# Kernel tuning notes

Measured on AMD Instinct MI355X. Metric: run time of the kernel, lower is better.

Reference implementation:

```python
import jax, jax.numpy as jnp
import numpy as np

B, S, H, DH, HQ, HKV = 2, 1024, 2048, 128, 16, 4
E, K, I, IS = 16, 4, 1024, 1024
EPS = 1e-5
ROPE_BASE = 10000.0
ROUTED_SCALE = 1.0


def rmsnorm(x, w):
    v = jnp.mean(x.astype(jnp.float32) ** 2, axis=-1, keepdims=True)
    return (x.astype(jnp.float32) * jax.lax.rsqrt(v + EPS)).astype(x.dtype) * w


def rope(x, cos, sin):
    x1, x2 = jnp.split(x, 2, axis=-1)
    return jnp.concatenate([x1 * cos - x2 * sin, x2 * cos + x1 * sin], axis=-1)


def setup_inputs() -> dict:
    key = jax.random.key(0)
    ks = jax.random.split(key, 24)
    s = 0.02
    inp = {}
    inp['x'] = jax.random.normal(ks[0], (B, S, H), dtype=jnp.float32)
    inp['in_ln_w'] = jnp.ones((H,), jnp.float32)
    inp['wq'] = jax.random.normal(ks[1], (H, HQ * DH), jnp.float32) * s
    inp['bq'] = jax.random.normal(ks[2], (HQ * DH,), jnp.float32) * s
    inp['wk'] = jax.random.normal(ks[3], (H, HKV * DH), jnp.float32) * s
    inp['bk'] = jax.random.normal(ks[4], (HKV * DH,), jnp.float32) * s
    inp['wv'] = jax.random.normal(ks[5], (H, HKV * DH), jnp.float32) * s
    inp['bv'] = jax.random.normal(ks[6], (HKV * DH,), jnp.float32) * s
    inp['qn_w'] = jnp.ones((DH,), jnp.float32)
    inp['kn_w'] = jnp.ones((DH,), jnp.float32)
    inp['wo'] = jax.random.normal(ks[7], (HQ * DH, H), jnp.float32) * s
    inp['post_ln_w'] = jnp.ones((H,), jnp.float32)
    inp['gate_w'] = jax.random.normal(ks[8], (E, H), jnp.float32) * s
    inp['gate_b'] = jax.random.normal(ks[9], (E,), jnp.float32) * s
    inp['wg'] = jax.random.normal(ks[10], (E, H, I), jnp.float32) * s
    inp['wu'] = jax.random.normal(ks[11], (E, H, I), jnp.float32) * s
    inp['wd'] = jax.random.normal(ks[12], (E, I, H), jnp.float32) * s
    inp['swg'] = jax.random.normal(ks[13], (H, IS), jnp.float32) * s
    inp['swu'] = jax.random.normal(ks[14], (H, IS), jnp.float32) * s
    inp['swd'] = jax.random.normal(ks[15], (IS, H), jnp.float32) * s
    return inp


def reference(x, in_ln_w, wq, bq, wk, bk, wv, bv, qn_w, kn_w, wo, post_ln_w,
              gate_w, gate_b, wg, wu, wd, swg, swu, swd):
    # ---- attention block ----
    res = x
    h = rmsnorm(x, in_ln_w)
    q = (h @ wq + bq).reshape(B, S, HQ, DH)
    k = (h @ wk + bk).reshape(B, S, HKV, DH)
    v = (h @ wv + bv).reshape(B, S, HKV, DH)
    q = rmsnorm(q, qn_w)  # per-head QK norm over head_dim
    k = rmsnorm(k, kn_w)
    inv_freq = 1.0 / (ROPE_BASE ** (jnp.arange(0, DH, 2, dtype=jnp.float32) / DH))  # [DH/2]
    fr = jnp.arange(S, dtype=jnp.float32)[:, None] * inv_freq[None, :]  # [S, DH/2]
    cos = jnp.cos(fr)[None, :, None, :]
    sin = jnp.sin(fr)[None, :, None, :]
    q = rope(q, cos, sin)
    k = rope(k, cos, sin)
    g = HQ // HKV
    k = jnp.repeat(k, g, axis=2)  # GQA expand to [B,S,HQ,DH]
    v = jnp.repeat(v, g, axis=2)
    scores = jnp.einsum('bqhd,bkhd->bhqk', q, k) * (DH ** -0.5)
    causal = jnp.tril(jnp.ones((S, S), dtype=bool))
    scores = jnp.where(causal[None, None], scores, jnp.float32(-1e30))
    attn = jax.nn.softmax(scores, axis=-1)
    o = jnp.einsum('bhqk,bkhd->bqhd', attn, v).reshape(B, S, HQ * DH) @ wo
    x = res + o
    # ---- MoE block ----
    res = x
    h = rmsnorm(x, post_ln_w)
    ht = h.reshape(B * S, H)  # [T, H]
    logits = ht.astype(jnp.float32) @ gate_w.T  # fp32 router
    scr = jax.nn.sigmoid(logits)  # [T, E]
    choice = scr + gate_b[None, :]  # noaux_tc: bias only for selection
    _, topi = jax.lax.top_k(choice, K)  # [T, K]
    tw = jnp.take_along_axis(scr, topi, axis=-1)  # unbiased combine weights
    tw = tw / (jnp.sum(tw, axis=-1, keepdims=True) + 1e-20)  # norm_topk_prob
    tw = tw * ROUTED_SCALE
    cw = jnp.sum(jax.nn.one_hot(topi, E, dtype=jnp.float32) * tw[..., None], axis=1)  # [T, E]
    a = jnp.einsum('th,ehi->eti', ht, wg)
    b = jnp.einsum('th,ehi->eti', ht, wu)
    inter = jax.nn.silu(a) * b * cw.T[:, :, None]  # scale before down-proj
    routed = jnp.einsum('eti,eih->th', inter, wd)
    shared = (jax.nn.silu(ht @ swg) * (ht @ swu)) @ swd
    out = res + (routed + shared).reshape(B, S, H)
    return out
```

## Files before the change

kernel.cpp:

```cpp
#include <hip/hip_runtime.h>
#include <math.h>

typedef unsigned short u16;
typedef __attribute__((ext_vector_type(8))) short short8;
typedef __attribute__((ext_vector_type(4))) float f32x4;

#define B_ 2
#define S_ 1024
#define H_ 2048
#define DH_ 128
#define HQ_ 16
#define HKV_ 4
#define E_ 16
#define TOPK_ 4
#define I_ 1024
#define T_ (B_*S_)
#define NQKV_ 3072
#define NSEG_ 17
#define NA_ (T_*TOPK_ + T_)
#define K3_ 6144

#define QPLANE ((long)B_*HQ_*S_*DH_)
#define KPLANE ((long)B_*HKV_*S_*DH_)
#define VPLANE ((long)B_*HKV_*DH_*S_)

__device__ __forceinline__ float bf2f(u16 u){
  union { unsigned int i; float f; } x; x.i = ((unsigned int)u) << 16; return x.f;
}
__device__ __forceinline__ u16 f2bf(float f){
  union { float f; unsigned int i; } x; x.f = f;
  unsigned int r = x.i + 0x7fffu + ((x.i >> 16) & 1u);
  return (u16)(r >> 16);
}
__device__ __forceinline__ void split_bf(float v, u16& hi, u16& lo){
  hi = f2bf(v);
  lo = f2bf(v - bf2f(hi));
}

__device__ __forceinline__ void gld_lds16(const void* g, void* l){
  __builtin_amdgcn_global_load_lds(
      (const __attribute__((address_space(1))) unsigned int*)g,
      (__attribute__((address_space(3))) unsigned int*)l, 16, 0, 0);
}

__device__ __forceinline__ f32x4 mfma_bf16(short8 a, short8 b, f32x4 c){
  return __builtin_amdgcn_mfma_f32_16x16x32_bf16(a, b, c, 0, 0, 0);
}

__global__ void k_transpose(const float* __restrict__ in, u16* __restrict__ out,
                            int R, int C, int rowMul, int rowOff,
                            long inBatch, long outBatch, int split3)
{
  __shared__ float tile[32][33];
  const float* inp = in + (long)blockIdx.z * inBatch;
  u16* outp = out + (long)blockIdx.z * outBatch;
  int c0 = blockIdx.x * 32, r0 = blockIdx.y * 32;
  int tx = threadIdx.x, ty = threadIdx.y;
#pragma unroll
  for (int i = 0; i < 4; i++)
    tile[ty*4+i][tx] = inp[(long)(r0 + ty*4 + i) * C + c0 + tx];
  __syncthreads();
#pragma unroll
  for (int i = 0; i < 4; i++){
    int c = c0 + ty*4 + i;
    float v = tile[tx][ty*4+i];
    if (split3){
      u16 hi, lo; split_bf(v, hi, lo);
      long base = (long)(c*rowMul + rowOff) * (3*R);
      outp[base + r0 + tx]       = hi;
      outp[base + R + r0 + tx]   = lo;
      outp[base + 2*R + r0 + tx] = hi;
    } else {
      outp[(long)(c*rowMul + rowOff) * R + r0 + tx] = f2bf(v);
    }
  }
}

__global__ void k_rmsnorm(const float* __restrict__ x, const float* __restrict__ w,
                          u16* __restrict__ out3, u16* __restrict__ out1,
                          float* __restrict__ outf)
{
  int t = blockIdx.x;
  const float4* r4 = (const float4*)(x + (long)t * H_);
  const float4* w4 = (const float4*)w;
  float4 a = r4[threadIdx.x], b = r4[threadIdx.x + 256];
  float ss = a.x*a.x + a.y*a.y + a.z*a.z + a.w*a.w
           + b.x*b.x + b.y*b.y + b.z*b.z + b.w*b.w;
#pragma unroll
  for (int d = 1; d < 64; d <<= 1) ss += __shfl_xor(ss, d);
  __shared__ float red[4];
  int lane = threadIdx.x & 63, wv = threadIdx.x >> 6;
  if (lane == 0) red[wv] = ss;
  __syncthreads();
  ss = red[0] + red[1] + red[2] + red[3];
  float rs = rsqrtf(ss * (1.f / 2048.f) + 1e-5f);
  float4 wa = w4[threadIdx.x], wb = w4[threadIdx.x + 256];
  float va[8] = { a.x*rs*wa.x, a.y*rs*wa.y, a.z*rs*wa.z, a.w*rs*wa.w,
                  b.x*rs*wb.x, b.y*rs*wb.y, b.z*rs*wb.z, b.w*rs*wb.w };
  int pos0 = threadIdx.x*4, pos1 = 1024 + threadIdx.x*4;
  if (out3){
    ushort4 hi0, lo0, hi1, lo1;
    split_bf(va[0], hi0.x, lo0.x); split_bf(va[1], hi0.y, lo0.y);
    split_bf(va[2], hi0.z, lo0.z); split_bf(va[3], hi0.w, lo0.w);
    split_bf(va[4], hi1.x, lo1.x); split_bf(va[5], hi1.y, lo1.y);
    split_bf(va[6], hi1.z, lo1.z); split_bf(va[7], hi1.w, lo1.w);
    u16* row = out3 + (long)t * K3_;
    *(ushort4*)(row + pos0) = hi0;        *(ushort4*)(row + pos1) = hi1;
    *(ushort4*)(row + 2048 + pos0) = hi0; *(ushort4*)(row + 2048 + pos1) = hi1;
    *(ushort4*)(row + 4096 + pos0) = lo0; *(ushort4*)(row + 4096 + pos1) = lo1;
  }
  if (out1){
    ushort4 p0 = { f2bf(va[0]), f2bf(va[1]), f2bf(va[2]), f2bf(va[3]) };
    ushort4 p1 = { f2bf(va[4]), f2bf(va[5]), f2bf(va[6]), f2bf(va[7]) };
    *(ushort4*)(out1 + (long)t*H_ + pos0) = p0;
    *(ushort4*)(out1 + (long)t*H_ + pos1) = p1;
  }
  if (outf){
    float4 oa = { va[0], va[1], va[2], va[3] };
    float4 ob = { va[4], va[5], va[6], va[7] };
    *(float4*)(outf + (long)t*H_ + pos0) = oa;
    *(float4*)(outf + (long)t*H_ + pos1) = ob;
  }
}

__global__ void k_ropetab(float* __restrict__ tab){
  int s = blockIdx.x, i = threadIdx.x;
  double inv = pow(10000.0, -(double)i / 64.0);
  double fr = (double)s * inv;
  tab[s*128 + i]      = (float)cos(fr);
  tab[s*128 + 64 + i] = (float)sin(fr);
}

__global__ void k_ropenorm(const float* __restrict__ qkv, const float* __restrict__ qnw,
                           const float* __restrict__ knw, const float* __restrict__ tab,
                           u16* __restrict__ Q, u16* __restrict__ Kn, u16* __restrict__ Vt)
{
  long gw = (long)blockIdx.x * 4 + (threadIdx.x >> 6);
  int lane = threadIdx.x & 63;
  int hr = (int)(gw % 24);
  long bs = gw / 24;
  int s = (int)(bs % S_);
  int b = (int)(bs / S_);
  const float* row = qkv + bs * NQKV_ + hr * DH_;
  float x1 = row[lane], x2 = row[lane + 64];
  if (hr < 20){
    float ss = x1*x1 + x2*x2;
#pragma unroll
    for (int d = 1; d < 64; d <<= 1) ss += __shfl_xor(ss, d);
    float rs = rsqrtf(ss * (1.f/128.f) + 1e-5f);
    const float* wn = (hr < 16) ? qnw : knw;
    float y1 = x1 * rs * wn[lane], y2 = x2 * rs * wn[lane + 64];
    float c = tab[s*128 + lane], sn = tab[s*128 + 64 + lane];
    float o1 = y1*c - y2*sn, o2 = y2*c + y1*sn;
    if (hr < 16){
      const float sc = 0.088388347648318447f;
      u16 h1,l1,h2,l2;
      split_bf(o1*sc, h1, l1); split_bf(o2*sc, h2, l2);
      u16* dst = Q + (((long)b*HQ_ + hr)*S_ + s) * DH_;
      dst[lane] = h1; dst[lane+64] = h2;
      dst[QPLANE + lane] = l1; dst[QPLANE + lane+64] = l2;
    } else {
      u16 h1,l1,h2,l2;
      split_bf(o1, h1, l1); split_bf(o2, h2, l2);
      u16* dst = Kn + (((long)b*HKV_ + (hr-16))*S_ + s) * DH_;
      dst[lane] = h1; dst[lane+64] = h2;
      dst[KPLANE + lane] = l1; dst[KPLANE + lane+64] = l2;
    }
  } else {
    u16 h1,l1,h2,l2;
    split_bf(x1, h1, l1); split_bf(x2, h2, l2);
    u16* dst = Vt + (((long)b*HKV_ + (hr-20))*DH_) * S_ + s;
    dst[(long)lane * S_]        = h1;
    dst[(long)(lane + 64) * S_] = h2;
    dst[VPLANE + (long)lane * S_]        = l1;
    dst[VPLANE + (long)(lane + 64) * S_] = l2;
  }
}

__launch_bounds__(256)
__global__ void k_attn(const u16* __restrict__ Q, const u16* __restrict__ Kn,
                       const u16* __restrict__ Vt, u16* __restrict__ O3)
{
  __shared__ u16 Ksh[32][128];
  __shared__ u16 Ksl[32][128];
  __shared__ u16 Vsh[128][32];
  __shared__ u16 Vsl[128][32];
  __shared__ u16 Psh[4][16][40];
  __shared__ u16 Psl[4][16][40];
  int qb = blockIdx.x, h = blockIdx.y, b = blockIdx.z;
  int kvh = h >> 2;
  int q0 = qb * 64;
  int tid = threadIdx.x, lane = tid & 63, w = tid >> 6;

  const u16* Qg = Q  + (((long)b*HQ_  + h  )*S_ + q0) * DH_;
  const u16* Kg = Kn + (((long)b*HKV_ + kvh)*S_) * DH_;
  const u16* Vg = Vt + (((long)b*HKV_ + kvh)*DH_) * S_;

  short8 qh[4], ql[4];
  {
    long qrow = w*16 + (lane & 15);
    int coff = (lane >> 4) << 3;
#pragma unroll
    for (int kst = 0; kst < 4; kst++){
      qh[kst] = *(const short8*)(Qg + qrow*DH_ + kst*32 + coff);
      ql[kst] = *(const short8*)(Qg + QPLANE + qrow*DH_ + kst*32 + coff);
    }
  }

  f32x4 o[8];
#pragma unroll
  for (int nt = 0; nt < 8; nt++) o[nt] = (f32x4){0.f,0.f,0.f,0.f};
  float mrow[4] = {-INFINITY,-INFINITY,-INFINITY,-INFINITY};
  float lrow[4] = {0.f,0.f,0.f,0.f};

  for (int j = 0; j <= 2*qb + 1; ++j){
#pragma unroll
    for (int it = 0; it < 2; ++it){
      int flat = it*256 + tid;
      int r = flat >> 4, pc = flat & 15;
      int c = pc ^ (((r&7) << 1) | ((r >> 3) & 1));
      long gsrc = ((long)(j*32 + r))*DH_ + c*8;
      gld_lds16(Kg + gsrc,          &Ksh[0][0] + (it*256 + (w<<6))*8);
      gld_lds16(Kg + KPLANE + gsrc, &Ksl[0][0] + (it*256 + (w<<6))*8);
    }
#pragma unroll
    for (int it = 0; it < 2; ++it){
      int flat = it*256 + tid;
      int r = flat >> 2, pc = flat & 3;
      int c = pc ^ (r & 3);
      long gsrc = (long)r*S_ + j*32 + c*8;
      gld_lds16(Vg + gsrc,          &Vsh[0][0] + (it*256 + (w<<6))*8);
      gld_lds16(Vg + VPLANE + gsrc, &Vsl[0][0] + (it*256 + (w<<6))*8);
    }
    __syncthreads();

    f32x4 s[2];
#pragma unroll
    for (int nt = 0; nt < 2; nt++) s[nt] = (f32x4){0.f,0.f,0.f,0.f};
#pragma unroll
    for (int kst = 0; kst < 4; kst++){
#pragma unroll
      for (int nt = 0; nt < 2; nt++){
        int br = nt*16 + (lane & 15);
        int bc = (kst*4 + (lane >> 4)) ^ (((br&7)<<1) | ((br>>3)&1));
        short8 kh = *(const short8*)&Ksh[br][bc*8];
        short8 kl = *(const short8*)&Ksl[br][bc*8];
        s[nt] = mfma_bf16(qh[kst], kh, s[nt]);
        s[nt] = mfma_bf16(qh[kst], kl, s[nt]);
        s[nt] = mfma_bf16(ql[kst], kh, s[nt]);
      }
    }
    if (j >= 2*qb){
#pragma unroll
      for (int nt = 0; nt < 2; nt++){
        int key = j*32 + nt*16 + (lane & 15);
#pragma unroll
        for (int r = 0; r < 4; r++){
          int qrow = q0 + w*16 + ((lane >> 4) << 2) + r;
          if (key > qrow) s[nt][r] = -1e30f;
        }
      }
    }
    float pm[4];
#pragma unroll
    for (int r = 0; r < 4; r++) pm[r] = fmaxf(s[0][r], s[1][r]);
#pragma unroll
    for (int d = 1; d < 16; d <<= 1){
#pragma unroll
      for (int r = 0; r < 4; r++) pm[r] = fmaxf(pm[r], __shfl_xor(pm[r], d));
    }
    float alpha[4];
#pragma unroll
    for (int r = 0; r < 4; r++){
      float mn = fmaxf(mrow[r], pm[r]);
      alpha[r] = __expf(mrow[r] - mn);
      mrow[r] = mn;
    }
    float psum[4] = {0.f,0.f,0.f,0.f};
#pragma unroll
    for (int nt = 0; nt < 2; nt++){
#pragma unroll
      for (int r = 0; r < 4; r++){
        float p = __expf(s[nt][r] - mrow[r]);
        psum[r] += p;
        u16 ph, pl; split_bf(p, ph, pl);
        int qr = ((lane>>4)<<2) + r, kc = nt*16 + (lane & 15);
        Psh[w][qr][kc] = ph;
        Psl[w][qr][kc] = pl;
      }
    }
#pragma unroll
    for (int d = 1; d < 16; d <<= 1){
#pragma unroll
      for (int r = 0; r < 4; r++) psum[r] += __shfl_xor(psum[r], d);
    }
#pragma unroll
    for (int r = 0; r < 4; r++) lrow[r] = lrow[r]*alpha[r] + psum[r];
#pragma unroll
    for (int nt = 0; nt < 8; nt++)
#pragma unroll
      for (int r = 0; r < 4; r++) o[nt][r] *= alpha[r];

    {
      short8 pah = *(const short8*)&Psh[w][lane & 15][(lane >> 4) << 3];
      short8 pal = *(const short8*)&Psl[w][lane & 15][(lane >> 4) << 3];
#pragma unroll
      for (int nt = 0; nt < 8; nt++){
        int br = nt*16 + (lane & 15);
        int bc = (lane >> 4) ^ (br & 3);
        short8 vh = *(const short8*)&Vsh[br][bc*8];
        short8 vl = *(const short8*)&Vsl[br][bc*8];
        o[nt] = mfma_bf16(pah, vh, o[nt]);
        o[nt] = mfma_bf16(pah, vl, o[nt]);
        o[nt] = mfma_bf16(pal, vh, o[nt]);
      }
    }
    __syncthreads();
  }
  float inv_[4];
#pragma unroll
  for (int r = 0; r < 4; r++) inv_[r] = 1.f / lrow[r];
#pragma unroll
  for (int nt = 0; nt < 8; nt++){
#pragma unroll
    for (int r = 0; r < 4; r++){
      long row = (long)b*S_ + q0 + w*16 + ((lane >> 4) << 2) + r;
      float val = o[nt][r] * inv_[r];
      u16 hi, lo; split_bf(val, hi, lo);
      long base = row*K3_ + h*DH_ + nt*16 + (lane & 15);
      O3[base]        = hi;
      O3[base + 2048] = hi;
      O3[base + 4096] = lo;
    }
  }
}

template<int MODE>
__launch_bounds__(256)
__global__ void k_gemm(const u16* __restrict__ A, const u16* __restrict__ Bm,
                       void* __restrict__ Cout, const float* __restrict__ aux0,
                       int M, int N, int K, long segStrideB,
                       const int* __restrict__ segStart, const int* __restrict__ segCount,
                       const int* __restrict__ assignTS, const float* __restrict__ assignW,
                       u16* __restrict__ downb)
{
  __shared__ u16 As[128][64];
  __shared__ u16 Bs[128][64];
  int tid = threadIdx.x;
  int lane = tid & 63, w = tid >> 6;
  int wr = w >> 1, wc = w & 1;
  int m0 = blockIdx.y * 128, n0 = blockIdx.x * 128;
  int seg = blockIdx.z;
  int segBase = 0, cnt = M;
  if constexpr (MODE >= 2){
    segBase = segStart[seg];
    cnt = segCount[seg];
    if (m0 >= cnt) return;
  }
  const u16* Bp = Bm + (long)seg * segStrideB;

  const u16* aS[4]; const u16* bS[4];
#pragma unroll
  for (int it = 0; it < 4; ++it){
    int flat = it*256 + tid;
    int r = flat >> 3, pc = flat & 7;
    int c = pc ^ (r & 7);
    long arow;
    if constexpr (MODE == 2) arow = (long)(assignTS[segBase + m0 + r] >> 3);
    else if constexpr (MODE == 3) arow = (long)(segBase + m0 + r);
    else arow = (long)(m0 + r);
    aS[it] = A + arow * K + c*8;
    bS[it] = Bp + (long)(n0 + r) * K + c*8;
  }

  f32x4 acc[4][4];
#pragma unroll
  for (int m = 0; m < 4; m++)
#pragma unroll
    for (int n = 0; n < 4; n++) acc[m][n] = (f32x4){0.f,0.f,0.f,0.f};

  u16* AsF = &As[0][0]; u16* BsF = &Bs[0][0];
  for (int k0 = 0; k0 < K; k0 += 64){
#pragma unroll
    for (int it = 0; it < 4; ++it){
      gld_lds16(aS[it] + k0, AsF + (it*256 + (w<<6))*8);
      gld_lds16(bS[it] + k0, BsF + (it*256 + (w<<6))*8);
    }
    __syncthreads();
#pragma unroll
    for (int kh = 0; kh < 2; ++kh){
      short8 af[4], bfv[4];
#pragma unroll
      for (int m = 0; m < 4; m++){
        int r = wr*64 + m*16 + (lane & 15);
        int c = (kh*4 + (lane >> 4)) ^ (r & 7);
        af[m] = *(const short8*)&As[r][c*8];
      }
#pragma unroll
      for (int n = 0; n < 4; n++){
        int r = wc*64 + n*16 + (lane & 15);
        int c = (kh*4 + (lane >> 4)) ^ (r & 7);
        bfv[n] = *(const short8*)&Bs[r][c*8];
      }
#pragma unroll
      for (int m = 0; m < 4; m++)
#pragma unroll
        for (int n = 0; n < 4; n++)
          acc[m][n] = mfma_bf16(af[m], bfv[n], acc[m][n]);
    }
    __syncthreads();
  }

  if constexpr (MODE == 0 || MODE == 1){
    float* C = (float*)Cout;
#pragma unroll
    for (int m = 0; m < 4; m++){
      int row0 = m0 + wr*64 + m*16 + ((lane >> 4) << 2);
#pragma unroll
      for (int n = 0; n < 4; n++){
        int col = n0 + wc*64 + n*16 + (lane & 15);
        float badd = (MODE == 0) ? aux0[col] : 0.f;
#pragma unroll
        for (int r = 0; r < 4; r++){
          float v = acc[m][n][r] + badd;
          if constexpr (MODE == 1) v += aux0[(long)(row0 + r)*N + col];
          C[(long)(row0 + r)*N + col] = v;
        }
      }
    }
  } else if constexpr (MODE == 2){
    u16* inter = (u16*)Cout;
#pragma unroll
    for (int m = 0; m < 4; m++){
      int row0 = m0 + wr*64 + m*16 + ((lane >> 4) << 2);
#pragma unroll
      for (int n = 0; n < 4; n++){
        f32x4 a = acc[m][n];
        float ov[4];
#pragma unroll
        for (int r = 0; r < 4; r++) ov[r] = __shfl_xor(a[r], 1);
        if ((lane & 1) == 0){
          int colp = (n0 + wc*64 + n*16 + (lane & 15)) >> 1;
#pragma unroll
          for (int r = 0; r < 4; r++){
            int rl = row0 + r;
            if (rl < cnt){
              int pos = segBase + rl;
              float g = a[r], u = ov[r];
              float val = (g / (1.f + __expf(-g))) * u * assignW[pos];
              inter[(long)pos*I_ + colp] = f2bf(val);
            }
          }
        }
      }
    }
  } else {
#pragma unroll
    for (int m = 0; m < 4; m++){
      int row0 = m0 + wr*64 + m*16 + ((lane >> 4) << 2);
#pragma unroll
      for (int n = 0; n < 4; n++){
        int col = n0 + wc*64 + n*16 + (lane & 15);
#pragma unroll
        for (int r = 0; r < 4; r++){
          int rl = row0 + r;
          if (rl < cnt){
            int ts = assignTS[segBase + rl];
            downb[((long)(ts >> 3)*5 + (ts & 7))*H_ + col] = f2bf(acc[m][n][r]);
          }
        }
      }
    }
  }
}

__global__ void k_router(const float* __restrict__ ht, const float* __restrict__ gw,
                         const float* __restrict__ gb, int* __restrict__ tok_e,
                         float* __restrict__ tok_w, int* __restrict__ counts)
{
  int t = blockIdx.x;
  const float* row = ht + (long)t * H_;
  int lane = threadIdx.x & 63, w = threadIdx.x >> 6;
  __shared__ float logits[16];
#pragma unroll
  for (int ei = 0; ei < 4; ei++){
    int e = w*4 + ei;
    const float* g = gw + (long)e * H_;
    float p = 0.f;
    for (int i = lane; i < H_; i += 64) p += row[i] * g[i];
#pragma unroll
    for (int d = 1; d < 64; d <<= 1) p += __shfl_xor(p, d);
    if (lane == 0) logits[e] = p;
  }
  __syncthreads();
  if (threadIdx.x == 0){
    float scr[16], ch[16];
#pragma unroll
    for (int e = 0; e < 16; e++){
      float s = 1.f / (1.f + __expf(-logits[e]));
      scr[e] = s; ch[e] = s + gb[e];
    }
    int sel[4]; float tw[4]; float sum = 0.f;
#pragma unroll
    for (int k = 0; k < 4; k++){
      int best = -1; float bv = -1e30f;
      for (int e = 0; e < 16; e++){
        bool used = false;
        for (int j = 0; j < k; j++) if (sel[j] == e) used = true;
        if (!used && ch[e] > bv){ bv = ch[e]; best = e; }
      }
      sel[k] = best; tw[k] = scr[best]; sum += scr[best];
    }
    float inv = 1.f / (sum + 1e-20f);
#pragma unroll
    for (int k = 0; k < 4; k++){
      tok_e[t*4 + k] = sel[k];
      tok_w[t*4 + k] = tw[k] * inv;
      atomicAdd(&counts[sel[k]], 1);
    }
  }
}

__global__ void k_scan(const int* __restrict__ counts, int* __restrict__ segStart,
                       int* __restrict__ segCount, int* __restrict__ cursor)
{
  if (threadIdx.x == 0){
    int off = 0;
    for (int e = 0; e < 16; e++){
      segStart[e] = off; segCount[e] = counts[e]; cursor[e] = off;
      off += counts[e];
    }
    segStart[16] = T_*TOPK_; segCount[16] = T_;
  }
}

__global__ void k_scatter(const int* __restrict__ tok_e, const float* __restrict__ tok_w,
                          int* __restrict__ cursor, int* __restrict__ assignTS,
                          float* __restrict__ assignW)
{
  int t = blockIdx.x*256 + threadIdx.x;
  if (t < T_){
    for (int k = 0; k < 4; k++){
      int e = tok_e[t*4 + k];
      int pos = atomicAdd(&cursor[e], 1);
      assignTS[pos] = t*8 + k;
      assignW[pos] = tok_w[t*4 + k];
    }
    assignTS[T_*TOPK_ + t] = t*8 + 4;
    assignW[T_*TOPK_ + t] = 1.f;
  }
}

__global__ void k_final(const float* __restrict__ xa, const u16* __restrict__ downb,
                        float* __restrict__ out)
{
  long i = ((long)blockIdx.x*256 + threadIdx.x) * 4;
  int t = (int)(i >> 11);
  int h = (int)(i & 2047);
  float4 r = *(const float4*)(xa + i);
  float a0 = r.x, a1 = r.y, a2 = r.z, a3 = r.w;
#pragma unroll
  for (int k = 0; k < 5; k++){
    const u16* d = downb + ((long)t*5 + k)*H_ + h;
    ushort4 v = *(const ushort4*)d;
    a0 += bf2f(v.x); a1 += bf2f(v.y); a2 += bf2f(v.z); a3 += bf2f(v.w);
  }
  float4 o = { a0, a1, a2, a3 };
  *(float4*)(out + i) = o;
}

extern "C" void kernel_launch(void* const* d_in, const int* in_sizes, int n_in,
                              void* d_out, int out_size, void* d_ws, size_t ws_size,
                              hipStream_t stream)
{
  (void)in_sizes; (void)n_in; (void)out_size; (void)ws_size;
  const float* x      = (const float*)d_in[0];
  const float* inlnw  = (const float*)d_in[1];
  const float* wq     = (const float*)d_in[2];
  const float* bq     = (const float*)d_in[3];
  const float* wk     = (const float*)d_in[4];
  const float* bk     = (const float*)d_in[5];
  const float* wv     = (const float*)d_in[6];
  const float* bv     = (const float*)d_in[7];
  const float* qnw    = (const float*)d_in[8];
  const float* knw    = (const float*)d_in[9];
  const float* wo     = (const float*)d_in[10];
  const float* postln = (const float*)d_in[11];
  const float* gatew  = (const float*)d_in[12];
  const float* gateb  = (const float*)d_in[13];
  const float* wg     = (const float*)d_in[14];
  const float* wu     = (const float*)d_in[15];
  const float* wdp    = (const float*)d_in[16];
  const float* swg    = (const float*)d_in[17];
  const float* swu    = (const float*)d_in[18];
  const float* swd    = (const float*)d_in[19];
  float* out = (float*)d_out;

  char* ws = (char*)d_ws;
  size_t off = 0;
  auto alloc = [&](size_t bytes) -> char* {
    char* p = ws + off; off += (bytes + 255) & ~(size_t)255; return p;
  };
  u16*   h2      = (u16*)  alloc((size_t)T_*K3_*2);
  u16*   wqkv2   = (u16*)  alloc((size_t)NQKV_*K3_*2);
  float* biascat = (float*)alloc((size_t)NQKV_*4);
  float* qkv     = (float*)alloc((size_t)T_*NQKV_*4);
  float* tab     = (float*)alloc((size_t)S_*128*4);
  u16*   Qb2     = (u16*)  alloc((size_t)2*QPLANE*2);
  u16*   Kn2     = (u16*)  alloc((size_t)2*KPLANE*2);
  u16*   Vt2     = (u16*)  alloc((size_t)2*VPLANE*2);
  u16*   wo2     = (u16*)  alloc((size_t)H_*K3_*2);
  float* xa      = (float*)alloc((size_t)T_*H_*4);
  u16*   ht_b    = (u16*)  alloc((size_t)T_*H_*2);
  u16*   wgu_t   = (u16*)  alloc((size_t)NSEG_*2048*2048*2);
  u16*   wd_t    = (u16*)  alloc((size_t)NSEG_*2048*1024*2);
  u16*   downb   = (u16*)  alloc((size_t)T_*5*H_*2);
  int*   tok_e   = (int*)  alloc((size_t)T_*4*4);
  float* tok_w   = (float*)alloc((size_t)T_*4*4);
  int*   counts  = (int*)  alloc(32*4);
  int*   segStart= (int*)  alloc(32*4);
  int*   segCount= (int*)  alloc(32*4);
  int*   cursor  = (int*)  alloc(32*4);
  int*   assignTS= (int*)  alloc((size_t)NA_*4);
  float* assignW = (float*)alloc((size_t)NA_*4);
  u16*   attno2  = (u16*)qkv;
  float* ht_f    = (float*)Qb2;
  u16*   inter   = h2;

  dim3 tb(32, 8);
  k_transpose<<<dim3(64,64,1),  tb, 0, stream>>>(wq,  wqkv2, 2048, 2048, 1, 0,    0, 0, 1);
  k_transpose<<<dim3(16,64,1),  tb, 0, stream>>>(wk,  wqkv2, 2048, 512,  1, 2048, 0, 0, 1);
  k_transpose<<<dim3(16,64,1),  tb, 0, stream>>>(wv,  wqkv2, 2048, 512,  1, 2560, 0, 0, 1);
  k_transpose<<<dim3(64,64,1),  tb, 0, stream>>>(wo,  wo2,   2048, 2048, 1, 0,    0, 0, 1);
  k_transpose<<<dim3(32,64,16), tb, 0, stream>>>(wg,  wgu_t, 2048, 1024, 2, 0, (long)2048*1024, (long)2048*2048, 0);
  k_transpose<<<dim3(32,64,16), tb, 0, stream>>>(wu,  wgu_t, 2048, 1024, 2, 1, (long)2048*1024, (long)2048*2048, 0);
  k_transpose<<<dim3(32,64,1),  tb, 0, stream>>>(swg, wgu_t + (long)16*2048*2048, 2048, 1024, 2, 0, 0, 0, 0);
  k_transpose<<<dim3(32,64,1),  tb, 0, stream>>>(swu, wgu_t + (long)16*2048*2048, 2048, 1024, 2, 1, 0, 0, 0);
  k_transpose<<<dim3(64,32,16), tb, 0, stream>>>(wdp, wd_t,  1024, 2048, 1, 0, (long)1024*2048, (long)2048*1024, 0);
  k_transpose<<<dim3(64,32,1),  tb, 0, stream>>>(swd, wd_t + (long)16*2048*1024, 1024, 2048, 1, 0, 0, 0, 0);

  hipMemcpyAsync(biascat,        bq, 2048*4, hipMemcpyDeviceToDevice, stream);
  hipMemcpyAsync(biascat + 2048, bk, 512*4,  hipMemcpyDeviceToDevice, stream);
  hipMemcpyAsync(biascat + 2560, bv, 512*4,  hipMemcpyDeviceToDevice, stream);

  k_ropetab<<<S_, 64, 0, stream>>>(tab);
  k_rmsnorm<<<T_, 256, 0, stream>>>(x, inlnw, h2, nullptr, nullptr);

  k_gemm<0><<<dim3(24,16,1), 256, 0, stream>>>(h2, wqkv2, qkv, biascat,
      T_, NQKV_, K3_, 0, nullptr, nullptr, nullptr, nullptr, nullptr);

  k_ropenorm<<<(T_*24)/4, 256, 0, stream>>>(qkv, qnw, knw, tab, Qb2, Kn2, Vt2);

  k_attn<<<dim3(S_/64, HQ_, B_), 256, 0, stream>>>(Qb2, Kn2, Vt2, attno2);

  k_gemm<1><<<dim3(16,16,1), 256, 0, stream>>>(attno2, wo2, xa, x,
      T_, H_, K3_, 0, nullptr, nullptr, nullptr, nullptr, nullptr);

  k_rmsnorm<<<T_, 256, 0, stream>>>(xa, postln, nullptr, ht_b, ht_f);

  hipMemsetAsync(counts, 0, 32*4, stream);
  k_router<<<T_, 256, 0, stream>>>(ht_f, gatew, gateb, tok_e, tok_w, counts);
  k_scan<<<1, 64, 0, stream>>>(counts, segStart, segCount, cursor);
  k_scatter<<<(T_+255)/256, 256, 0, stream>>>(tok_e, tok_w, cursor, assignTS, assignW);

  k_gemm<2><<<dim3(16,16,NSEG_), 256, 0, stream>>>(ht_b, wgu_t, inter, nullptr,
      0, 2048, H_, (long)2048*2048, segStart, segCount, assignTS, assignW, nullptr);

  k_gemm<3><<<dim3(16,16,NSEG_), 256, 0, stream>>>(inter, wd_t, nullptr, nullptr,
      0, H_, I_, (long)2048*1024, segStart, segCount, assignTS, assignW, downb);

  k_final<<<(T_*H_/4)/256, 256, 0, stream>>>(xa, downb, out);
}
```

Measured before the change: 978.3 us.

## Split-K dense GEMMs, compact MoE tile list, fuse residual add into post-norm

The QKV and output-projection GEMMs now use split-K (2 and 3 slices) so their small 16x24 / 16x16 grids gain more blocks. The fp32 partials are summed later: bias is added in ropenorm, and the residual add is fused into a new add+rmsnorm kernel. The grouped MoE GEMMs launch from a compact tile list built in the scan kernel, replacing a 16x16x17 grid where most blocks exited early. This costs extra fp32 partial-buffer traffic and reworks the workspace aliasing.

```diff
diff --git a/kernel.cpp b/kernel.cpp
--- a/kernel.cpp
+++ b/kernel.cpp
@@ -19,6 +19,7 @@
 #define NSEG_ 17
 #define NA_ (T_*TOPK_ + T_)
 #define K3_ 6144
+#define MAXTILE 97
 
 #define QPLANE ((long)B_*HQ_*S_*DH_)
 #define KPLANE ((long)B_*HKV_*S_*DH_)
@@ -77,8 +78,7 @@
 }
 
 __global__ void k_rmsnorm(const float* __restrict__ x, const float* __restrict__ w,
-                          u16* __restrict__ out3, u16* __restrict__ out1,
-                          float* __restrict__ outf)
+                          u16* __restrict__ out3)
 {
   int t = blockIdx.x;
   const float4* r4 = (const float4*)(x + (long)t * H_);
@@ -98,29 +98,62 @@
   float va[8] = { a.x*rs*wa.x, a.y*rs*wa.y, a.z*rs*wa.z, a.w*rs*wa.w,
                   b.x*rs*wb.x, b.y*rs*wb.y, b.z*rs*wb.z, b.w*rs*wb.w };
   int pos0 = threadIdx.x*4, pos1 = 1024 + threadIdx.x*4;
-  if (out3){
-    ushort4 hi0, lo0, hi1, lo1;
-    split_bf(va[0], hi0.x, lo0.x); split_bf(va[1], hi0.y, lo0.y);
-    split_bf(va[2], hi0.z, lo0.z); split_bf(va[3], hi0.w, lo0.w);
-    split_bf(va[4], hi1.x, lo1.x); split_bf(va[5], hi1.y, lo1.y);
-    split_bf(va[6], hi1.z, lo1.z); split_bf(va[7], hi1.w, lo1.w);
-    u16* row = out3 + (long)t * K3_;
-    *(ushort4*)(row + pos0) = hi0;        *(ushort4*)(row + pos1) = hi1;
-    *(ushort4*)(row + 2048 + pos0) = hi0; *(ushort4*)(row + 2048 + pos1) = hi1;
-    *(ushort4*)(row + 4096 + pos0) = lo0; *(ushort4*)(row + 4096 + pos1) = lo1;
-  }
-  if (out1){
-    ushort4 p0 = { f2bf(va[0]), f2bf(va[1]), f2bf(va[2]), f2bf(va[3]) };
-    ushort4 p1 = { f2bf(va[4]), f2bf(va[5]), f2bf(va[6]), f2bf(va[7]) };
-    *(ushort4*)(out1 + (long)t*H_ + pos0) = p0;
-    *(ushort4*)(out1 + (long)t*H_ + pos1) = p1;
-  }
-  if (outf){
-    float4 oa = { va[0], va[1], va[2], va[3] };
-    float4 ob = { va[4], va[5], va[6], va[7] };
-    *(float4*)(outf + (long)t*H_ + pos0) = oa;
-    *(float4*)(outf + (long)t*H_ + pos1) = ob;
-  }
+  ushort4 hi0, lo0, hi1, lo1;
+  split_bf(va[0], hi0.x, lo0.x); split_bf(va[1], hi0.y, lo0.y);
+  split_bf(va[2], hi0.z, lo0.z); split_bf(va[3], hi0.w, lo0.w);
+  split_bf(va[4], hi1.x, lo1.x); split_bf(va[5], hi1.y, lo1.y);
+  split_bf(va[6], hi1.z, lo1.z); split_bf(va[7], hi1.w, lo1.w);
+  u16* row = out3 + (long)t * K3_;
+  *(ushort4*)(row + pos0) = hi0;        *(ushort4*)(row + pos1) = hi1;
+  *(ushort4*)(row + 2048 + pos0) = hi0; *(ushort4*)(row + 2048 + pos1) = hi1;
+  *(ushort4*)(row + 4096 + pos0) = lo0; *(ushort4*)(row + 4096 + pos1) = lo1;
+}
+
+__global__ void k_add_rmsnorm(const float* __restrict__ x, const float* __restrict__ p0,
+                              const float* __restrict__ p1, const float* __restrict__ p2,
+                              const float* __restrict__ w, float* __restrict__ xa,
+                              u16* __restrict__ out1, float* __restrict__ outf)
+{
+  int t = blockIdx.x;
+  long base = (long)t * H_;
+  const float4* x4 = (const float4*)(x + base);
+  const float4* a4 = (const float4*)(p0 + base);
+  const float4* b4 = (const float4*)(p1 + base);
+  const float4* c4 = (const float4*)(p2 + base);
+  const float4* w4 = (const float4*)w;
+  int i0 = threadIdx.x, i1 = threadIdx.x + 256;
+  float4 xv0 = x4[i0], xv1 = x4[i1];
+  float4 av0 = a4[i0], av1 = a4[i1];
+  float4 bv0 = b4[i0], bv1 = b4[i1];
+  float4 cv0 = c4[i0], cv1 = c4[i1];
+  float4 s0, s1;
+  s0.x = xv0.x+av0.x+bv0.x+cv0.x; s0.y = xv0.y+av0.y+bv0.y+cv0.y;
+  s0.z = xv0.z+av0.z+bv0.z+cv0.z; s0.w = xv0.w+av0.w+bv0.w+cv0.w;
+  s1.x = xv1.x+av1.x+bv1.x+cv1.x; s1.y = xv1.y+av1.y+bv1.y+cv1.y;
+  s1.z = xv1.z+av1.z+bv1.z+cv1.z; s1.w = xv1.w+av1.w+bv1.w+cv1.w;
+  *(float4*)(xa + base + i0*4) = s0;
+  *(float4*)(xa + base + i1*4) = s1;
+  float ss = s0.x*s0.x + s0.y*s0.y + s0.z*s0.z + s0.w*s0.w
+           + s1.x*s1.x + s1.y*s1.y + s1.z*s1.z + s1.w*s1.w;
+#pragma unroll
+  for (int d = 1; d < 64; d <<= 1) ss += __shfl_xor(ss, d);
+  __shared__ float red[4];
+  int lane = threadIdx.x & 63, wv = threadIdx.x >> 6;
+  if (lane == 0) red[wv] = ss;
+  __syncthreads();
+  ss = red[0] + red[1] + red[2] + red[3];
+  float rs = rsqrtf(ss * (1.f / 2048.f) + 1e-5f);
+  float4 wa = w4[i0], wb = w4[i1];
+  float va[8] = { s0.x*rs*wa.x, s0.y*rs*wa.y, s0.z*rs*wa.z, s0.w*rs*wa.w,
+                  s1.x*rs*wb.x, s1.y*rs*wb.y, s1.z*rs*wb.z, s1.w*rs*wb.w };
+  ushort4 q0 = { f2bf(va[0]), f2bf(va[1]), f2bf(va[2]), f2bf(va[3]) };
+  ushort4 q1 = { f2bf(va[4]), f2bf(va[5]), f2bf(va[6]), f2bf(va[7]) };
+  *(ushort4*)(out1 + base + i0*4) = q0;
+  *(ushort4*)(out1 + base + i1*4) = q1;
+  float4 oa = { va[0], va[1], va[2], va[3] };
+  float4 ob = { va[4], va[5], va[6], va[7] };
+  *(float4*)(outf + base + i0*4) = oa;
+  *(float4*)(outf + base + i1*4) = ob;
 }
 
 __global__ void k_ropetab(float* __restrict__ tab){
@@ -131,8 +164,10 @@
   tab[s*128 + 64 + i] = (float)sin(fr);
 }
 
-__global__ void k_ropenorm(const float* __restrict__ qkv, const float* __restrict__ qnw,
-                           const float* __restrict__ knw, const float* __restrict__ tab,
+__global__ void k_ropenorm(const float* __restrict__ qkv0, const float* __restrict__ qkv1,
+                           const float* __restrict__ biascat,
+                           const float* __restrict__ qnw, const float* __restrict__ knw,
+                           const float* __restrict__ tab,
                            u16* __restrict__ Q, u16* __restrict__ Kn, u16* __restrict__ Vt)
 {
   long gw = (long)blockIdx.x * 4 + (threadIdx.x >> 6);
@@ -141,8 +176,9 @@
   long bs = gw / 24;
   int s = (int)(bs % S_);
   int b = (int)(bs / S_);
-  const float* row = qkv + bs * NQKV_ + hr * DH_;
-  float x1 = row[lane], x2 = row[lane + 64];
+  long ro = bs * NQKV_ + hr * DH_;
+  float x1 = qkv0[ro + lane] + qkv1[ro + lane] + biascat[hr*DH_ + lane];
+  float x2 = qkv0[ro + lane + 64] + qkv1[ro + lane + 64] + biascat[hr*DH_ + lane + 64];
   if (hr < 20){
     float ss = x1*x1 + x2*x2;
 #pragma unroll
@@ -338,9 +374,11 @@
 template<int MODE>
 __launch_bounds__(256)
 __global__ void k_gemm(const u16* __restrict__ A, const u16* __restrict__ Bm,
-                       void* __restrict__ Cout, const float* __restrict__ aux0,
-                       int M, int N, int K, long segStrideB,
+                       void* __restrict__ Cout,
+                       int M, int N, int Kloop, int Kstride, long segStrideB,
                        const int* __restrict__ segStart, const int* __restrict__ segCount,
+                       const int* __restrict__ tileSeg, const int* __restrict__ tileMb,
+                       const int* __restrict__ meta,
                        const int* __restrict__ assignTS, const float* __restrict__ assignW,
                        u16* __restrict__ downb)
 {
@@ -349,13 +387,19 @@
   int tid = threadIdx.x;
   int lane = tid & 63, w = tid >> 6;
   int wr = w >> 1, wc = w & 1;
-  int m0 = blockIdx.y * 128, n0 = blockIdx.x * 128;
-  int seg = blockIdx.z;
-  int segBase = 0, cnt = M;
+  int n0 = blockIdx.x * 128;
+  int seg = 0, m0, segBase = 0, cnt = M, kbase = 0;
+  long outOff = 0;
   if constexpr (MODE >= 2){
+    int ty = blockIdx.y;
+    if (ty >= meta[0]) return;
+    seg = tileSeg[ty]; m0 = tileMb[ty] * 128;
     segBase = segStart[seg];
     cnt = segCount[seg];
-    if (m0 >= cnt) return;
+  } else {
+    m0 = blockIdx.y * 128;
+    kbase = blockIdx.z * Kloop;
+    outOff = (long)blockIdx.z * M * N;
   }
   const u16* Bp = Bm + (long)seg * segStrideB;
 
@@ -369,8 +413,8 @@
     if constexpr (MODE == 2) arow = (long)(assignTS[segBase + m0 + r] >> 3);
     else if constexpr (MODE == 3) arow = (long)(segBase + m0 + r);
     else arow = (long)(m0 + r);
-    aS[it] = A + arow * K + c*8;
-    bS[it] = Bp + (long)(n0 + r) * K + c*8;
+    aS[it] = A + arow * Kstride + kbase + c*8;
+    bS[it] = Bp + (long)(n0 + r) * Kstride + kbase + c*8;
   }
 
   f32x4 acc[4][4];
@@ -380,7 +424,7 @@
     for (int n = 0; n < 4; n++) acc[m][n] = (f32x4){0.f,0.f,0.f,0.f};
 
   u16* AsF = &As[0][0]; u16* BsF = &Bs[0][0];
-  for (int k0 = 0; k0 < K; k0 += 64){
+  for (int k0 = 0; k0 < Kloop; k0 += 64){
 #pragma unroll
     for (int it = 0; it < 4; ++it){
       gld_lds16(aS[it] + k0, AsF + (it*256 + (w<<6))*8);
@@ -412,20 +456,16 @@
   }
 
   if constexpr (MODE == 0 || MODE == 1){
-    float* C = (float*)Cout;
+    float* C = (float*)Cout + outOff;
 #pragma unroll
     for (int m = 0; m < 4; m++){
       int row0 = m0 + wr*64 + m*16 + ((lane >> 4) << 2);
 #pragma unroll
       for (int n = 0; n < 4; n++){
         int col = n0 + wc*64 + n*16 + (lane & 15);
-        float badd = (MODE == 0) ? aux0[col] : 0.f;
-#pragma unroll
-        for (int r = 0; r < 4; r++){
-          float v = acc[m][n][r] + badd;
-          if constexpr (MODE == 1) v += aux0[(long)(row0 + r)*N + col];
-          C[(long)(row0 + r)*N + col] = v;
-        }
+#pragma unroll
+        for (int r = 0; r < 4; r++)
+          C[(long)(row0 + r)*N + col] = acc[m][n][r];
       }
     }
   } else if constexpr (MODE == 2){
@@ -522,15 +562,20 @@
 }
 
 __global__ void k_scan(const int* __restrict__ counts, int* __restrict__ segStart,
-                       int* __restrict__ segCount, int* __restrict__ cursor)
+                       int* __restrict__ segCount, int* __restrict__ cursor,
+                       int* __restrict__ tileSeg, int* __restrict__ tileMb,
+                       int* __restrict__ meta)
 {
   if (threadIdx.x == 0){
-    int off = 0;
+    int off = 0, nt = 0;
     for (int e = 0; e < 16; e++){
       segStart[e] = off; segCount[e] = counts[e]; cursor[e] = off;
+      for (int mb = 0; mb*128 < counts[e]; ++mb){ tileSeg[nt] = e; tileMb[nt] = mb; nt++; }
       off += counts[e];
     }
     segStart[16] = T_*TOPK_; segCount[16] = T_;
+    for (int mb = 0; mb < 16; ++mb){ tileSeg[nt] = 16; tileMb[nt] = mb; nt++; }
+    meta[0] = nt;
   }
 }
 
@@ -601,31 +646,40 @@
   auto alloc = [&](size_t bytes) -> char* {
     char* p = ws + off; off += (bytes + 255) & ~(size_t)255; return p;
   };
-  u16*   h2      = (u16*)  alloc((size_t)T_*K3_*2);
   u16*   wqkv2   = (u16*)  alloc((size_t)NQKV_*K3_*2);
-  float* biascat = (float*)alloc((size_t)NQKV_*4);
-  float* qkv     = (float*)alloc((size_t)T_*NQKV_*4);
-  float* tab     = (float*)alloc((size_t)S_*128*4);
-  u16*   Qb2     = (u16*)  alloc((size_t)2*QPLANE*2);
-  u16*   Kn2     = (u16*)  alloc((size_t)2*KPLANE*2);
-  u16*   Vt2     = (u16*)  alloc((size_t)2*VPLANE*2);
   u16*   wo2     = (u16*)  alloc((size_t)H_*K3_*2);
-  float* xa      = (float*)alloc((size_t)T_*H_*4);
-  u16*   ht_b    = (u16*)  alloc((size_t)T_*H_*2);
   u16*   wgu_t   = (u16*)  alloc((size_t)NSEG_*2048*2048*2);
   u16*   wd_t    = (u16*)  alloc((size_t)NSEG_*2048*1024*2);
-  u16*   downb   = (u16*)  alloc((size_t)T_*5*H_*2);
+  float* tab     = (float*)alloc((size_t)S_*128*4);
+  float* biascat = (float*)alloc((size_t)NQKV_*4);
+  float* xa      = (float*)alloc((size_t)T_*H_*4);
   int*   tok_e   = (int*)  alloc((size_t)T_*4*4);
   float* tok_w   = (float*)alloc((size_t)T_*4*4);
   int*   counts  = (int*)  alloc(32*4);
   int*   segStart= (int*)  alloc(32*4);
   int*   segCount= (int*)  alloc(32*4);
   int*   cursor  = (int*)  alloc(32*4);
+  int*   tileSeg = (int*)  alloc(128*4);
+  int*   tileMb  = (int*)  alloc(128*4);
+  int*   meta    = (int*)  alloc(32*4);
   int*   assignTS= (int*)  alloc((size_t)NA_*4);
   float* assignW = (float*)alloc((size_t)NA_*4);
-  u16*   attno2  = (u16*)qkv;
-  float* ht_f    = (float*)Qb2;
-  u16*   inter   = h2;
+  char*  scrA    = alloc((size_t)T_*K3_*2);
+  char*  scrBC   = alloc((size_t)2*T_*NQKV_*4);
+  char*  scrD    = alloc((size_t)(2*QPLANE + 2*KPLANE + 2*VPLANE)*2);
+
+  u16*   h2      = (u16*)scrA;
+  u16*   attno2  = (u16*)scrA;
+  u16*   inter   = (u16*)scrA;
+  float* qkvp0   = (float*)scrBC;
+  float* qkvp1   = (float*)(scrBC + (size_t)T_*NQKV_*4);
+  float* wop     = (float*)scrBC;
+  u16*   Qb2     = (u16*)scrD;
+  u16*   Kn2     = (u16*)(scrD + (size_t)2*QPLANE*2);
+  u16*   Vt2     = (u16*)(scrD + (size_t)2*QPLANE*2 + (size_t)2*KPLANE*2);
+  float* ht_f    = (float*)scrD;
+  u16*   ht_b    = (u16*)(scrD + (size_t)T_*H_*4);
+  u16*   downb   = (u16*)scrD;
 
   dim3 tb(32, 8);
   k_transpose<<<dim3(64,64,1),  tb, 0, stream>>>(wq,  wqkv2, 2048, 2048, 1, 0,    0, 0, 1);
@@ -644,30 +698,31 @@
   hipMemcpyAsync(biascat + 2560, bv, 512*4,  hipMemcpyDeviceToDevice, stream);
 
   k_ropetab<<<S_, 64, 0, stream>>>(tab);
-  k_rmsnorm<<<T_, 256, 0, stream>>>(x, inlnw, h2, nullptr, nullptr);
-
-  k_gemm<0><<<dim3(24,16,1), 256, 0, stream>>>(h2, wqkv2, qkv, biascat,
-      T_, NQKV_, K3_, 0, nullptr, nullptr, nullptr, nullptr, nullptr);
-
-  k_ropenorm<<<(T_*24)/4, 256, 0, stream>>>(qkv, qnw, knw, tab, Qb2, Kn2, Vt2);
+  k_rmsnorm<<<T_, 256, 0, stream>>>(x, inlnw, h2);
+
+  k_gemm<0><<<dim3(24,16,2), 256, 0, stream>>>(h2, wqkv2, qkvp0, T_, NQKV_,
+      K3_/2, K3_, 0, nullptr, nullptr, nullptr, nullptr, nullptr, nullptr, nullptr, nullptr);
+
+  k_ropenorm<<<(T_*24)/4, 256, 0, stream>>>(qkvp0, qkvp1, biascat, qnw, knw, tab, Qb2, Kn2, Vt2);
 
   k_attn<<<dim3(S_/64, HQ_, B_), 256, 0, stream>>>(Qb2, Kn2, Vt2, attno2);
 
-  k_gemm<1><<<dim3(16,16,1), 256, 0, stream>>>(attno2, wo2, xa, x,
-      T_, H_, K3_, 0, nullptr, nullptr, nullptr, nullptr, nullptr);
-
-  k_rmsnorm<<<T_, 256, 0, stream>>>(xa, postln, nullptr, ht_b, ht_f);
+  k_gemm<1><<<dim3(16,16,3), 256, 0, stream>>>(attno2, wo2, wop, T_, H_,
+      K3_/3, K3_, 0, nullptr, nullptr, nullptr, nullptr, nullptr, nullptr, nullptr, nullptr);
+
+  k_add_rmsnorm<<<T_, 256, 0, stream>>>(x, wop, wop + (long)T_*H_, wop + (long)2*T_*H_,
+      postln, xa, ht_b, ht_f);
 
   hipMemsetAsync(counts, 0, 32*4, stream);
   k_router<<<T_, 256, 0, stream>>>(ht_f, gatew, gateb, tok_e, tok_w, counts);
-  k_scan<<<1, 64, 0, stream>>>(counts, segStart, segCount, cursor);
+  k_scan<<<1, 64, 0, stream>>>(counts, segStart, segCount, cursor, tileSeg, tileMb, meta);
   k_scatter<<<(T_+255)/256, 256, 0, stream>>>(tok_e, tok_w, cursor, assignTS, assignW);
 
-  k_gemm<2><<<dim3(16,16,NSEG_), 256, 0, stream>>>(ht_b, wgu_t, inter, nullptr,
-      0, 2048, H_, (long)2048*2048, segStart, segCount, assignTS, assignW, nullptr);
-
-  k_gemm<3><<<dim3(16,16,NSEG_), 256, 0, stream>>>(inter, wd_t, nullptr, nullptr,
-      0, H_, I_, (long)2048*1024, segStart, segCount, assignTS, assignW, downb);
+  k_gemm<2><<<dim3(16,MAXTILE,1), 256, 0, stream>>>(ht_b, wgu_t, inter, 0, 2048,
+      H_, H_, (long)2048*2048, segStart, segCount, tileSeg, tileMb, meta, assignTS, assignW, nullptr);
+
+  k_gemm<3><<<dim3(16,MAXTILE,1), 256, 0, stream>>>(inter, wd_t, nullptr, 0, H_,
+      I_, I_, (long)2048*1024, segStart, segCount, tileSeg, tileMb, meta, assignTS, assignW, downb);
 
   k_final<<<(T_*H_/4)/256, 256, 0, stream>>>(xa, downb, out);
 }
```

New measurement: 938.5 us. -4.1%, faster.
